# Performance work log

Hardware: AMD Instinct MI355X
Metric: run time of the kernel (lower is better)

Reference implementation:

```python
import jax, jax.numpy as jnp
import numpy as np

B, H, V, T = 1024, 512, 2048, 32  # batch, hidden_size, output_size (vocab), max_len


def setup_inputs() -> dict:
    key = jax.random.key(0)
    ks = jax.random.split(key, 8)
    s = 1.0 / np.sqrt(H)  # torch LSTMCell/Linear init scale
    u = lambda k, shp: jax.random.uniform(k, shp, jnp.float32, -s, s)
    return {
        "encoder_hidden": jax.random.normal(ks[0], (B, H), jnp.float32),
        "encoder_cell": jax.random.normal(ks[1], (B, H), jnp.float32),
        "W_ih": u(ks[2], (4 * H, V)),   # LSTMCell(output_size -> hidden)
        "W_hh": u(ks[3], (4 * H, H)),
        "b_ih": u(ks[4], (4 * H,)),
        "b_hh": u(ks[5], (4 * H,)),
        "W_out": u(ks[6], (V, H)),      # Linear(hidden -> output_size)
        "b_out": u(ks[7], (V,)),
        "init_input": jnp.zeros((1, V), jnp.float32),
        "max_len": T,
        "eos_idx": 0,
    }


def reference(encoder_hidden, encoder_cell, W_ih, W_hh, b_ih, b_hh, W_out, b_out,
              init_input, max_len, eos_idx):
    batch = encoder_hidden.shape[0]
    vocab = W_out.shape[0]
    hid = encoder_hidden.shape[1]

    def lstm_cell(x, h, c):
        gates = x @ W_ih.T + b_ih + h @ W_hh.T + b_hh  # [B, 4H]
        i, f, g, o = jnp.split(gates, 4, axis=1)       # torch gate order i,f,g,o
        c_new = jax.nn.sigmoid(f) * c + jax.nn.sigmoid(i) * jnp.tanh(g)
        h_new = jax.nn.sigmoid(o) * jnp.tanh(c_new)
        return h_new, c_new

    def step(carry, _):
        h, c, x, mask = carry
        h, c = lstm_cell(x, h, c)
        logit = h @ W_out.T + b_out                    # [B, V]
        # eval / non-msg path: hard argmax one-hot
        predict = jax.nn.one_hot(jnp.argmax(logit, axis=1), vocab, dtype=mask.dtype)
        new_mask = mask * (1.0 - predict[:, eos_idx])  # [1, B]
        # embedding is None -> decoder_input = predict
        return (h, c, predict, new_mask), (predict, logit, mask)

    carry0 = (
        encoder_hidden,
        encoder_cell,
        jnp.broadcast_to(init_input, (batch, vocab)),
        jnp.ones((1, batch), jnp.float32),
    )
    _, (predicts, logits, masks) = jax.lax.scan(step, carry0, None, length=max_len)
    return predicts, logits, masks  # [T,B,V], [T,B,V], [T,1,B]
```

## Files before the change

kernel.cpp:

```cpp
#include <hip/hip_runtime.h>
#include <math.h>

#define B_ 1024
#define H_ 512
#define V_ 2048
#define T_ 32
#define G_ 2048
#define KP 1024
#define K3 1536
#define NC 24

#define A_SCALE 64.0f
#define B_SCALE 256.0f
#define SCALE_INV (1.0f / (64.0f * 256.0f))

typedef _Float16 f16x8 __attribute__((ext_vector_type(8)));
typedef float f32x4 __attribute__((ext_vector_type(4)));

__device__ __forceinline__ float sigmoidf_(float x) {
    return 1.0f / (1.0f + expf(-x));
}

__device__ __forceinline__ void stage16(const _Float16* g, _Float16* l) {
#if __has_builtin(__builtin_amdgcn_global_load_lds)
    __builtin_amdgcn_global_load_lds(
        (const __attribute__((address_space(1))) void*)g,
        (__attribute__((address_space(3))) void*)l, 16, 0, 0);
#else
    *(uint4*)l = *(const uint4*)g;
#endif
}

__device__ __forceinline__ void wgbar() { asm volatile("s_barrier" ::: "memory"); }


__global__ __launch_bounds__(512, 2) void gemm1_fused(
    const _Float16* __restrict__ Hin,
    const _Float16* __restrict__ Wg,
    const float* __restrict__ bsum,
    const float* __restrict__ g0,
    const float* __restrict__ W_ihT,
    const float* __restrict__ W_ih,
    const int* __restrict__ idx,
    float* __restrict__ c,
    _Float16* __restrict__ Hout,
    int t, int modeA)
{
    __shared__ _Float16 As[2 * 2 * 128 * 32];
    __shared__ _Float16 Bs[2 * 2 * 64 * 32];
    const int tid = threadIdx.x;
    const int bm  = blockIdx.y * 128;
    const int bnj = blockIdx.x * 16;

    const int rB  = (tid & 255) >> 2;
    const int gcB = ((rB >> 4) << 9) + bnj + (rB & 15);
    const _Float16* aSrc = Hin + (size_t)(bm + (tid >> 2)) * KP + (tid & 3) * 8;
    const _Float16* bSrc = Wg  + (size_t)gcB * KP + (tid >> 8) * 32 + (tid & 3) * 8;
    _Float16* aDst = As + tid * 8;
    _Float16* bDst = Bs + (tid >> 8) * 2048 + (tid & 255) * 8;

    const int w    = tid >> 6;
    const int wr   = w >> 1;
    const int wc   = w & 1;
    const int lane = tid & 63;
    const int l15  = lane & 15;
    const int kq   = lane >> 4;

    f32x4 acc[2][2];
#pragma unroll
    for (int mt = 0; mt < 2; ++mt)
#pragma unroll
        for (int g = 0; g < 2; ++g) acc[mt][g] = (f32x4){0.f, 0.f, 0.f, 0.f};

    auto STAGE = [&](int buf, int ch) {
        const int kk = ch * 64;
        const int aoff = (kk < 512) ? kk : kk - 512;
        const int boff = (kk < 1024) ? kk : kk - 1024;
#pragma unroll
        for (int ks = 0; ks < 2; ++ks)
            stage16(aSrc + aoff + ks * 32, aDst + buf * 8192 + ks * 4096);
        stage16(bSrc + boff, bDst + buf * 4096);
    };

    int cur = 0;
    STAGE(0, 0);
    for (int ch = 0; ch < NC; ++ch) {
        if (ch + 1 < NC) {
            STAGE(cur ^ 1, ch + 1);
            asm volatile("s_waitcnt vmcnt(3)" ::: "memory");
        } else {
            asm volatile("s_waitcnt vmcnt(0)" ::: "memory");
        }
        wgbar();
#pragma unroll
        for (int ks = 0; ks < 2; ++ks) {
            const _Float16* ab = As + cur * 8192 + ks * 4096;
            const _Float16* bb = Bs + cur * 4096 + ks * 2048;
            f16x8 a0 = *(const f16x8*)&ab[(wr * 32 + l15) * 32 + kq * 8];
            f16x8 a1 = *(const f16x8*)&ab[(wr * 32 + 16 + l15) * 32 + kq * 8];
#pragma unroll
            for (int g = 0; g < 2; ++g) {
                f16x8 b = *(const f16x8*)&bb[((wc * 2 + g) * 16 + l15) * 32 + kq * 8];
                acc[0][g] = __builtin_amdgcn_mfma_f32_16x16x32_f16(a0, b, acc[0][g], 0, 0, 0);
                acc[1][g] = __builtin_amdgcn_mfma_f32_16x16x32_f16(a1, b, acc[1][g], 0, 0, 0);
            }
        }
        wgbar();
        cur ^= 1;
    }

    float* sc    = (float*)As;
    float* sc_go = sc;
    float* sc_if = sc + 2048;
#pragma unroll
    for (int rg = 0; rg < 4; ++rg) {
        const int rl = wr * 16 + kq * 4 + rg;
        if (wc == 1) {
            sc_go[(rl * 16 + l15) * 2 + 0] = acc[0][0][rg];
            sc_go[(rl * 16 + l15) * 2 + 1] = acc[0][1][rg];
        } else {
            sc_if[(rl * 16 + l15) * 2 + 0] = acc[1][0][rg];
            sc_if[(rl * 16 + l15) * 2 + 1] = acc[1][1][rg];
        }
    }
    __syncthreads();

    const int j = bnj + l15;
    const float bs0 = bsum[j];
    const float bs1 = bsum[512 + j];
    const float bs2 = bsum[1024 + j];
    const float bs3 = bsum[1536 + j];
#pragma unroll
    for (int rg = 0; rg < 4; ++rg) {
        const int rl  = wr * 16 + kq * 4 + rg;
        const int row = bm + wr * 32 + wc * 16 + kq * 4 + rg;
        float ai, af, ag, ao;
        if (wc == 0) {
            ai = acc[0][0][rg]; af = acc[0][1][rg];
            ag = sc_go[(rl * 16 + l15) * 2 + 0];
            ao = sc_go[(rl * 16 + l15) * 2 + 1];
        } else {
            ai = sc_if[(rl * 16 + l15) * 2 + 0];
            af = sc_if[(rl * 16 + l15) * 2 + 1];
            ag = acc[1][0][rg]; ao = acc[1][1][rg];
        }
        float xg0, xg1, xg2, xg3;
        if (t == 0) {
            xg0 = g0[j]; xg1 = g0[512 + j]; xg2 = g0[1024 + j]; xg3 = g0[1536 + j];
        } else if (modeA) {
            const float* xr = W_ihT + (size_t)idx[row] * G_;
            xg0 = xr[j]; xg1 = xr[512 + j]; xg2 = xr[1024 + j]; xg3 = xr[1536 + j];
        } else {
            const int v = idx[row];
            xg0 = W_ih[(size_t)(j) * V_ + v];
            xg1 = W_ih[(size_t)(512 + j) * V_ + v];
            xg2 = W_ih[(size_t)(1024 + j) * V_ + v];
            xg3 = W_ih[(size_t)(1536 + j) * V_ + v];
        }
        const float gi = ai * SCALE_INV + bs0 + xg0;
        const float gf = af * SCALE_INV + bs1 + xg1;
        const float gg = ag * SCALE_INV + bs2 + xg2;
        const float go = ao * SCALE_INV + bs3 + xg3;
        const float co = c[(size_t)row * H_ + j];
        const float cn = sigmoidf_(gf) * co + sigmoidf_(gi) * tanhf(gg);
        const float hn = sigmoidf_(go) * tanhf(cn);
        c[(size_t)row * H_ + j] = cn;
        const float hs = A_SCALE * hn;
        const _Float16 hi = (_Float16)hs;
        const _Float16 lo = (_Float16)(hs - (float)hi);
        Hout[(size_t)row * KP + j] = hi;
        Hout[(size_t)row * KP + 512 + j] = lo;
    }
}

__global__ __launch_bounds__(512, 2) void gemm2_fused(
    const _Float16* __restrict__ Hin,
    const _Float16* __restrict__ Wo,
    const float* __restrict__ b_out,
    float* __restrict__ logits,
    float* __restrict__ pval,
    int* __restrict__ pidx)
{
    __shared__ _Float16 As[2 * 2 * 64 * 32];
    __shared__ _Float16 Bs[2 * 2 * 128 * 32];
    const int tid = threadIdx.x;
    const int bm = blockIdx.y * 64;
    const int bn = blockIdx.x * 128;

    const _Float16* aSrc = Hin + (size_t)(bm + ((tid & 255) >> 2)) * KP + (tid & 3) * 8;
    const _Float16* bSrc = Wo  + (size_t)(bn + (tid >> 2)) * KP + (tid & 3) * 8;
    _Float16* aDst = As + (tid >> 8) * 2048 + (tid & 255) * 8;
    _Float16* bDst = Bs + tid * 8;

    const int w    = tid >> 6;
    const int wm   = w & 1;
    const int wn   = w >> 1;
    const int lane = tid & 63;
    const int l15  = lane & 15;
    const int kq   = lane >> 4;

    f32x4 acc[2][2];
#pragma unroll
    for (int mt = 0; mt < 2; ++mt)
#pragma unroll
        for (int nt = 0; nt < 2; ++nt) acc[mt][nt] = (f32x4){0.f, 0.f, 0.f, 0.f};

    auto STAGE = [&](int buf, int ch) {
        const int kk = ch * 64;
        const int aoff = (kk < 512) ? kk : kk - 512;
        const int boff = (kk < 1024) ? kk : kk - 1024;
        stage16(aSrc + aoff + (tid >> 8) * 32, aDst + buf * 4096);
#pragma unroll
        for (int ks = 0; ks < 2; ++ks)
            stage16(bSrc + boff + ks * 32, bDst + buf * 8192 + ks * 4096);
    };

    int cur = 0;
    STAGE(0, 0);
    for (int ch = 0; ch < NC; ++ch) {
        if (ch + 1 < NC) {
            STAGE(cur ^ 1, ch + 1);
            asm volatile("s_waitcnt vmcnt(3)" ::: "memory");
        } else {
            asm volatile("s_waitcnt vmcnt(0)" ::: "memory");
        }
        wgbar();
#pragma unroll
        for (int ks = 0; ks < 2; ++ks) {
            const _Float16* ab = As + cur * 4096 + ks * 2048;
            const _Float16* bb = Bs + cur * 8192 + ks * 4096;
            f16x8 a0 = *(const f16x8*)&ab[(wm * 32 + l15) * 32 + kq * 8];
            f16x8 a1 = *(const f16x8*)&ab[(wm * 32 + 16 + l15) * 32 + kq * 8];
#pragma unroll
            for (int nt = 0; nt < 2; ++nt) {
                f16x8 b = *(const f16x8*)&bb[((wn * 32 + nt * 16) + l15) * 32 + kq * 8];
                acc[0][nt] = __builtin_amdgcn_mfma_f32_16x16x32_f16(a0, b, acc[0][nt], 0, 0, 0);
                acc[1][nt] = __builtin_amdgcn_mfma_f32_16x16x32_f16(a1, b, acc[1][nt], 0, 0, 0);
            }
        }
        wgbar();
        cur ^= 1;
    }

    const int c0 = bn + wn * 32 + l15;
    const int c1 = c0 + 16;
    const float bo0 = b_out[c0];
    const float bo1 = b_out[c1];
    const int cid = blockIdx.x * 4 + wn;
#pragma unroll
    for (int mt = 0; mt < 2; ++mt) {
#pragma unroll
        for (int rg = 0; rg < 4; ++rg) {
            const int row = bm + wm * 32 + mt * 16 + kq * 4 + rg;
            const float v0 = acc[mt][0][rg] * SCALE_INV + bo0;
            const float v1 = acc[mt][1][rg] * SCALE_INV + bo1;
            float* lrow = logits + (size_t)row * V_;
            lrow[c0] = v0; lrow[c1] = v1;
            float bv; int bc;
            if (v1 > v0) { bv = v1; bc = c1; } else { bv = v0; bc = c0; }
#pragma unroll
            for (int off = 1; off < 16; off <<= 1) {
                const float ov = __shfl_xor(bv, off, 64);
                const int   oc = __shfl_xor(bc, off, 64);
                if (ov > bv || (ov == bv && oc < bc)) { bv = ov; bc = oc; }
            }
            if (l15 == 0) { pval[row * 64 + cid] = bv; pidx[row * 64 + cid] = bc; }
        }
    }
}

__global__ __launch_bounds__(256) void finalize_step(
    const float* __restrict__ pval, const int* __restrict__ pidx,
    float* __restrict__ predicts_t, float* __restrict__ masks_t,
    float* __restrict__ mask, int* __restrict__ idx,
    const int* __restrict__ eos_idx)
{
    const int row  = blockIdx.x * 4 + (threadIdx.x >> 6);
    const int lane = threadIdx.x & 63;
    float bv = pval[row * 64 + lane];
    int   bc = pidx[row * 64 + lane];
#pragma unroll
    for (int off = 1; off < 64; off <<= 1) {
        const float ov = __shfl_xor(bv, off, 64);
        const int   oc = __shfl_xor(bc, off, 64);
        if (ov > bv || (ov == bv && oc < bc)) { bv = ov; bc = oc; }
    }
    if (lane == 0) {
        idx[row] = bc;
        predicts_t[(size_t)row * V_ + bc] = 1.0f;
        masks_t[row] = mask[row];
        if (bc == *eos_idx) mask[row] = 0.0f;
    }
}

__global__ __launch_bounds__(256) void prep_misc(
    const float* __restrict__ eh, const float* __restrict__ ec,
    const float* __restrict__ b_ih, const float* __restrict__ b_hh,
    _Float16* __restrict__ hA, float* __restrict__ c,
    float* __restrict__ bsum, float* __restrict__ mask)
{
    const int gid = blockIdx.x * 256 + threadIdx.x;
    const int row = gid >> 9;
    const int j   = gid & 511;
    const float x = eh[gid];
    c[gid] = ec[gid];
    const float xs = A_SCALE * x;
    const _Float16 hi = (_Float16)xs;
    const _Float16 lo = (_Float16)(xs - (float)hi);
    hA[(size_t)row * KP + j] = hi;
    hA[(size_t)row * KP + 512 + j] = lo;
    if (gid < G_) bsum[gid] = b_ih[gid] + b_hh[gid];
    if (gid < B_) mask[gid] = 1.0f;
}

__global__ __launch_bounds__(256) void prep_w(
    const float* __restrict__ W_hh, const float* __restrict__ W_out,
    _Float16* __restrict__ Wg, _Float16* __restrict__ Wo)
{
    const int gid = blockIdx.x * 256 + threadIdx.x;
    const int sel = gid >> 20;
    const int i   = gid & 1048575;
    const int n   = i >> 9;
    const int k   = i & 511;
    const float ws = (sel ? W_out[i] : W_hh[i]) * B_SCALE;
    const _Float16 hi = (_Float16)ws;
    const _Float16 lo = (_Float16)(ws - (float)hi);
    _Float16* dst = sel ? Wo : Wg;
    dst[(size_t)n * KP + k] = hi;
    dst[(size_t)n * KP + 512 + k] = lo;
}

__global__ __launch_bounds__(256) void transpose2048(const float* __restrict__ in,
                                                     float* __restrict__ out)
{
    __shared__ float tile[32][33];
    const int bx = blockIdx.x * 32;
    const int by = blockIdx.y * 32;
    const int tx = threadIdx.x & 31;
    const int ty = threadIdx.x >> 5;
#pragma unroll
    for (int i = 0; i < 32; i += 8)
        tile[ty + i][tx] = in[(size_t)(by + ty + i) * V_ + bx + tx];
    __syncthreads();
#pragma unroll
    for (int i = 0; i < 32; i += 8)
        out[(size_t)(bx + ty + i) * G_ + by + tx] = tile[tx][ty + i];
}

__global__ __launch_bounds__(256) void g0_kernel(const float* __restrict__ init_input,
                                                 const float* __restrict__ W_ih,
                                                 float* __restrict__ g0)
{
    const int gc   = blockIdx.x * 4 + (threadIdx.x >> 6);
    const int lane = threadIdx.x & 63;
    float acc = 0.0f;
    for (int v = lane; v < V_; v += 64) acc += init_input[v] * W_ih[(size_t)gc * V_ + v];
#pragma unroll
    for (int off = 32; off > 0; off >>= 1) acc += __shfl_down(acc, off, 64);
    if (lane == 0) g0[gc] = acc;
}

extern "C" void kernel_launch(void* const* d_in, const int* in_sizes, int n_in,
                              void* d_out, int out_size, void* d_ws, size_t ws_size,
                              hipStream_t stream) {
    const float* enc_h      = (const float*)d_in[0];
    const float* enc_c      = (const float*)d_in[1];
    const float* W_ih       = (const float*)d_in[2];
    const float* W_hh       = (const float*)d_in[3];
    const float* b_ih       = (const float*)d_in[4];
    const float* b_hh       = (const float*)d_in[5];
    const float* W_out      = (const float*)d_in[6];
    const float* b_out      = (const float*)d_in[7];
    const float* init_input = (const float*)d_in[8];
    const int*   eos_idx    = (const int*)d_in[10];

    float* out      = (float*)d_out;
    float* predicts = out;
    float* logits   = out + (size_t)T_ * B_ * V_;
    float* masks    = out + 2 * (size_t)T_ * B_ * V_;

    size_t off = 0;
    auto alloc = [&](size_t bytes) {
        void* p = (char*)d_ws + off;
        off += (bytes + 255) & ~(size_t)255;
        return p;
    };
    _Float16* Wg   = (_Float16*)alloc((size_t)G_ * KP * 2);
    _Float16* Wo   = (_Float16*)alloc((size_t)V_ * KP * 2);
    _Float16* hA   = (_Float16*)alloc((size_t)B_ * KP * 2);
    _Float16* hB   = (_Float16*)alloc((size_t)B_ * KP * 2);
    float*    c    = (float*)alloc((size_t)B_ * H_ * 4);
    float*    pval = (float*)alloc((size_t)B_ * 64 * 4);
    int*      pidx = (int*)alloc((size_t)B_ * 64 * 4);
    float*    g0   = (float*)alloc((size_t)G_ * 4);
    float*    bsum = (float*)alloc((size_t)G_ * 4);
    float*    mask = (float*)alloc((size_t)B_ * 4);
    int*      idx  = (int*)alloc((size_t)B_ * 4);
    float*    W_ihT = (float*)((char*)d_ws + off);
    const int modeA = (off + (size_t)V_ * G_ * 4) <= ws_size;

    hipMemsetAsync(predicts, 0, (size_t)T_ * B_ * V_ * sizeof(float), stream);
    prep_misc<<<(B_ * H_) / 256, 256, 0, stream>>>(enc_h, enc_c, b_ih, b_hh, hA, c, bsum, mask);
    prep_w<<<(2 * G_ * H_) / 256, 256, 0, stream>>>(W_hh, W_out, Wg, Wo);
    g0_kernel<<<G_ / 4, 256, 0, stream>>>(init_input, W_ih, g0);
    if (modeA)
        transpose2048<<<dim3(64, 64), 256, 0, stream>>>(W_ih, W_ihT);

    for (int t = 0; t < T_; ++t) {
        const _Float16* hin = (t & 1) ? hB : hA;
        _Float16*      hout = (t & 1) ? hA : hB;
        gemm1_fused<<<dim3(32, 8), 512, 0, stream>>>(
            hin, Wg, bsum, g0, W_ihT, W_ih, idx, c, hout, t, modeA);
        gemm2_fused<<<dim3(16, 16), 512, 0, stream>>>(
            hout, Wo, b_out, logits + (size_t)t * B_ * V_, pval, pidx);
        finalize_step<<<256, 256, 0, stream>>>(
            pval, pidx, predicts + (size_t)t * B_ * V_, masks + (size_t)t * B_,
            mask, idx, eos_idx);
    }
}
```

Before: 1.923 ms.

## Fuse argmax finalize into next-step LSTM gate kernel and prefetch gate inputs

Removes the per-step finalize_step launch by having gemm1_fused reduce the previous step's partial argmax results. Block column 0 writes the one-hot prediction and mask for the previous step, and a single finalize runs after the loop for the last step. The embedding-row gathers, the bias loads and the old cell state are now loaded before the MFMA loop so their latency overlaps the staged loads. The cost is a redundant argmax reduction in every one of the 32 column blocks and more live registers.

```diff
diff --git a/kernel.cpp b/kernel.cpp
--- a/kernel.cpp
+++ b/kernel.cpp
@@ -33,7 +33,6 @@
 
 __device__ __forceinline__ void wgbar() { asm volatile("s_barrier" ::: "memory"); }
 
-
 __global__ __launch_bounds__(512, 2) void gemm1_fused(
     const _Float16* __restrict__ Hin,
     const _Float16* __restrict__ Wg,
@@ -41,13 +40,19 @@
     const float* __restrict__ g0,
     const float* __restrict__ W_ihT,
     const float* __restrict__ W_ih,
-    const int* __restrict__ idx,
+    const float* __restrict__ pval,
+    const int* __restrict__ pidx,
+    float* __restrict__ predicts_tm1,
+    float* __restrict__ masks_tm1,
+    float* __restrict__ mask,
+    const int* __restrict__ eos_idx,
     float* __restrict__ c,
     _Float16* __restrict__ Hout,
     int t, int modeA)
 {
     __shared__ _Float16 As[2 * 2 * 128 * 32];
     __shared__ _Float16 Bs[2 * 2 * 64 * 32];
+    __shared__ int sIdx[128];
     const int tid = threadIdx.x;
     const int bm  = blockIdx.y * 128;
     const int bnj = blockIdx.x * 16;
@@ -66,12 +71,6 @@
     const int l15  = lane & 15;
     const int kq   = lane >> 4;
 
-    f32x4 acc[2][2];
-#pragma unroll
-    for (int mt = 0; mt < 2; ++mt)
-#pragma unroll
-        for (int g = 0; g < 2; ++g) acc[mt][g] = (f32x4){0.f, 0.f, 0.f, 0.f};
-
     auto STAGE = [&](int buf, int ch) {
         const int kk = ch * 64;
         const int aoff = (kk < 512) ? kk : kk - 512;
@@ -84,6 +83,71 @@
 
     int cur = 0;
     STAGE(0, 0);
+
+    if (t > 0) {
+        const int rloc = tid >> 2;
+        const int part = tid & 3;
+        const int rowg = bm + rloc;
+        float bv = -3.402823466e+38f;
+        int   bc = 0x7fffffff;
+        const float* pv = pval + rowg * 64 + part * 16;
+        const int*   pi = pidx + rowg * 64 + part * 16;
+#pragma unroll
+        for (int i2 = 0; i2 < 16; ++i2) {
+            const float v = pv[i2];
+            const int  ci = pi[i2];
+            if (v > bv || (v == bv && ci < bc)) { bv = v; bc = ci; }
+        }
+#pragma unroll
+        for (int off = 1; off < 4; off <<= 1) {
+            const float ov = __shfl_xor(bv, off, 64);
+            const int   oc = __shfl_xor(bc, off, 64);
+            if (ov > bv || (ov == bv && oc < bc)) { bv = ov; bc = oc; }
+        }
+        if (part == 0) {
+            sIdx[rloc] = bc;
+            if (blockIdx.x == 0) {
+                predicts_tm1[(size_t)rowg * V_ + bc] = 1.0f;
+                masks_tm1[rowg] = mask[rowg];
+                if (bc == *eos_idx) mask[rowg] = 0.0f;
+            }
+        }
+    }
+    __syncthreads();
+
+    const int j = bnj + l15;
+    const float bs0 = bsum[j];
+    const float bs1 = bsum[512 + j];
+    const float bs2 = bsum[1024 + j];
+    const float bs3 = bsum[1536 + j];
+    float xg0[4], xg1[4], xg2[4], xg3[4], cpre[4];
+#pragma unroll
+    for (int rg = 0; rg < 4; ++rg) {
+        const int rl2 = wr * 32 + wc * 16 + kq * 4 + rg;
+        const int row = bm + rl2;
+        cpre[rg] = c[(size_t)row * H_ + j];
+        if (t == 0) {
+            xg0[rg] = g0[j]; xg1[rg] = g0[512 + j];
+            xg2[rg] = g0[1024 + j]; xg3[rg] = g0[1536 + j];
+        } else if (modeA) {
+            const float* xr = W_ihT + (size_t)sIdx[rl2] * G_;
+            xg0[rg] = xr[j]; xg1[rg] = xr[512 + j];
+            xg2[rg] = xr[1024 + j]; xg3[rg] = xr[1536 + j];
+        } else {
+            const int v = sIdx[rl2];
+            xg0[rg] = W_ih[(size_t)(j) * V_ + v];
+            xg1[rg] = W_ih[(size_t)(512 + j) * V_ + v];
+            xg2[rg] = W_ih[(size_t)(1024 + j) * V_ + v];
+            xg3[rg] = W_ih[(size_t)(1536 + j) * V_ + v];
+        }
+    }
+
+    f32x4 acc[2][2];
+#pragma unroll
+    for (int mt = 0; mt < 2; ++mt)
+#pragma unroll
+        for (int g = 0; g < 2; ++g) acc[mt][g] = (f32x4){0.f, 0.f, 0.f, 0.f};
+
     for (int ch = 0; ch < NC; ++ch) {
         if (ch + 1 < NC) {
             STAGE(cur ^ 1, ch + 1);
@@ -125,11 +189,6 @@
     }
     __syncthreads();
 
-    const int j = bnj + l15;
-    const float bs0 = bsum[j];
-    const float bs1 = bsum[512 + j];
-    const float bs2 = bsum[1024 + j];
-    const float bs3 = bsum[1536 + j];
 #pragma unroll
     for (int rg = 0; rg < 4; ++rg) {
         const int rl  = wr * 16 + kq * 4 + rg;
@@ -144,24 +203,11 @@
             af = sc_if[(rl * 16 + l15) * 2 + 1];
             ag = acc[1][0][rg]; ao = acc[1][1][rg];
         }
-        float xg0, xg1, xg2, xg3;
-        if (t == 0) {
-            xg0 = g0[j]; xg1 = g0[512 + j]; xg2 = g0[1024 + j]; xg3 = g0[1536 + j];
-        } else if (modeA) {
-            const float* xr = W_ihT + (size_t)idx[row] * G_;
-            xg0 = xr[j]; xg1 = xr[512 + j]; xg2 = xr[1024 + j]; xg3 = xr[1536 + j];
-        } else {
-            const int v = idx[row];
-            xg0 = W_ih[(size_t)(j) * V_ + v];
-            xg1 = W_ih[(size_t)(512 + j) * V_ + v];
-            xg2 = W_ih[(size_t)(1024 + j) * V_ + v];
-            xg3 = W_ih[(size_t)(1536 + j) * V_ + v];
-        }
-        const float gi = ai * SCALE_INV + bs0 + xg0;
-        const float gf = af * SCALE_INV + bs1 + xg1;
-        const float gg = ag * SCALE_INV + bs2 + xg2;
-        const float go = ao * SCALE_INV + bs3 + xg3;
-        const float co = c[(size_t)row * H_ + j];
+        const float gi = ai * SCALE_INV + bs0 + xg0[rg];
+        const float gf = af * SCALE_INV + bs1 + xg1[rg];
+        const float gg = ag * SCALE_INV + bs2 + xg2[rg];
+        const float go = ao * SCALE_INV + bs3 + xg3[rg];
+        const float co = cpre[rg];
         const float cn = sigmoidf_(gf) * co + sigmoidf_(gi) * tanhf(gg);
         const float hn = sigmoidf_(go) * tanhf(cn);
         c[(size_t)row * H_ + j] = cn;
@@ -199,6 +245,11 @@
     const int l15  = lane & 15;
     const int kq   = lane >> 4;
 
+    const int c0 = bn + wn * 32 + l15;
+    const int c1 = c0 + 16;
+    const float bo0 = b_out[c0];
+    const float bo1 = b_out[c1];
+
     f32x4 acc[2][2];
 #pragma unroll
     for (int mt = 0; mt < 2; ++mt)
@@ -242,10 +293,6 @@
         cur ^= 1;
     }
 
-    const int c0 = bn + wn * 32 + l15;
-    const int c1 = c0 + 16;
-    const float bo0 = b_out[c0];
-    const float bo1 = b_out[c1];
     const int cid = blockIdx.x * 4 + wn;
 #pragma unroll
     for (int mt = 0; mt < 2; ++mt) {
@@ -409,12 +456,15 @@
     for (int t = 0; t < T_; ++t) {
         const _Float16* hin = (t & 1) ? hB : hA;
         _Float16*      hout = (t & 1) ? hA : hB;
+        const int tp = (t > 0) ? (t - 1) : 0;
         gemm1_fused<<<dim3(32, 8), 512, 0, stream>>>(
-            hin, Wg, bsum, g0, W_ihT, W_ih, idx, c, hout, t, modeA);
+            hin, Wg, bsum, g0, W_ihT, W_ih, pval, pidx,
+            predicts + (size_t)tp * B_ * V_, masks + (size_t)tp * B_,
+            mask, eos_idx, c, hout, t, modeA);
         gemm2_fused<<<dim3(16, 16), 512, 0, stream>>>(
             hout, Wo, b_out, logits + (size_t)t * B_ * V_, pval, pidx);
-        finalize_step<<<256, 256, 0, stream>>>(
-            pval, pidx, predicts + (size_t)t * B_ * V_, masks + (size_t)t * B_,
-            mask, idx, eos_idx);
-    }
-}
+    }
+    finalize_step<<<256, 256, 0, stream>>>(
+        pval, pidx, predicts + (size_t)(T_ - 1) * B_ * V_, masks + (size_t)(T_ - 1) * B_,
+        mask, idx, eos_idx);
+}
```

Result: slower. 2.083 ms (+8.3%).
